# Optimization experiments

Measured on AMD Instinct MI355X. Metric: run time of the kernel, lower is better.

## Reference

```python
import jax, jax.numpy as jnp
import numpy as np

C = 256          # channels
K = 7            # kernel_size
GC = 16          # group_channels (hardcoded in module)
G = C // GC      # groups = 16
RED = 4          # reduction_ratio
PAD = (K - 1) // 2
EPS = 1e-5


def _bn(x, gamma, beta, mean, var):
    # inference-mode BatchNorm2d over channel dim (axis=1)
    inv = gamma / jnp.sqrt(var + EPS)
    return x * inv[None, :, None, None] + (beta - mean * inv)[None, :, None, None]


def setup_inputs() -> dict:
    key = jax.random.key(0)
    ks = jax.random.split(key, 8)
    cm = C // RED  # 64
    x = jax.random.normal(ks[0], (4, C, 64, 64), dtype=jnp.float32)
    w1 = jax.random.normal(ks[1], (cm, C), dtype=jnp.float32) * (1.0 / np.sqrt(C))
    bn1_gamma = jnp.abs(jax.random.normal(ks[2], (cm,), dtype=jnp.float32)) + 0.5
    bn1_beta = jax.random.normal(ks[3], (cm,), dtype=jnp.float32) * 0.1
    bn1_mean = jnp.zeros((cm,), jnp.float32)
    bn1_var = jnp.ones((cm,), jnp.float32)
    w2 = jax.random.normal(ks[4], (K * K * G, cm), dtype=jnp.float32) * (1.0 / np.sqrt(cm))
    b2 = jax.random.normal(ks[5], (K * K * G,), dtype=jnp.float32) * 0.1
    bn2_gamma = jnp.abs(jax.random.normal(ks[6], (C,), dtype=jnp.float32)) + 0.5
    bn2_beta = jax.random.normal(ks[7], (C,), dtype=jnp.float32) * 0.1
    bn2_mean = jnp.zeros((C,), jnp.float32)
    bn2_var = jnp.ones((C,), jnp.float32)
    return {"x": x, "w1": w1, "bn1_gamma": bn1_gamma, "bn1_beta": bn1_beta,
            "bn1_mean": bn1_mean, "bn1_var": bn1_var, "w2": w2, "b2": b2,
            "bn2_gamma": bn2_gamma, "bn2_beta": bn2_beta,
            "bn2_mean": bn2_mean, "bn2_var": bn2_var}


def reference(x, w1, bn1_gamma, bn1_beta, bn1_mean, bn1_var,
              w2, b2, bn2_gamma, bn2_beta, bn2_mean, bn2_var):
    b, c, h, w = x.shape
    # weight branch: 1x1 conv (no bias) -> BN -> ReLU -> 1x1 conv (bias)
    t = jnp.einsum('oc,bchw->bohw', w1, x)
    t = jax.nn.relu(_bn(t, bn1_gamma, bn1_beta, bn1_mean, bn1_var))
    wgt = jnp.einsum('oc,bchw->bohw', w2, t) + b2[None, :, None, None]
    wgt = wgt.reshape(b, G, K * K, h, w)  # per-pixel kernel per group
    # unfold x: extract KxK patches (stride 1, pad PAD), torch ordering:
    # channel slowest, kernel row, kernel col fastest
    x_pad = jnp.pad(x, ((0, 0), (0, 0), (PAD, PAD), (PAD, PAD)))
    patches = jnp.stack([x_pad[:, :, i:i + h, j:j + w]
                         for i in range(K) for j in range(K)], axis=2)  # (b,c,K2,h,w)
    patches = patches.reshape(b, G, GC, K * K, h, w)
    out = jnp.einsum('bgckhw,bgkhw->bgchw', patches, wgt).reshape(b, c, h, w)
    return jax.nn.relu(_bn(out, bn2_gamma, bn2_beta, bn2_mean, bn2_var))
```

## Files before the change

### kernel.cpp

```cpp
#include <hip/hip_runtime.h>

#define BN 4
#define C 256
#define H 64
#define W 64
#define CM 64
#define G 16
#define GC 16
#define KS 7
#define K2 49
#define PADD 3
#define EPSV 1e-5f

#define TS 16
#define HSLOT_U 388

#define W1T_OFF 0
#define B2P_OFF (W1T_OFF + C*CM)
#define S1_OFF  (B2P_OFF + G*64)
#define B1_OFF  (S1_OFF + CM)
#define S2_OFF  (B1_OFF + CM)
#define B2C_OFF (S2_OFF + C)
#define ZERO_OFF (B2C_OFF + C)
#define ABF_OFF (ZERO_OFF + 16)
#define TBF_OFF (ABF_OFF + 32768)
#define XBF_OFF (TBF_OFF + 524288)

typedef __attribute__((ext_vector_type(8))) short bf16x8;
typedef __attribute__((ext_vector_type(4))) float f32x4;

__device__ __forceinline__ uint f2bf_rne(float f) {
  uint u = __float_as_uint(f);
  return (u + 0x7fffu + ((u >> 16) & 1u)) >> 16;
}

__device__ __forceinline__ void gload_lds4(const void* g, void* l) {
  __builtin_amdgcn_global_load_lds(
      (const __attribute__((address_space(1))) void*)g,
      (__attribute__((address_space(3))) void*)l, 4, 0, 0);
}

__global__ __launch_bounds__(256) void prep_kernel(
    const float* __restrict__ w1, const float* __restrict__ w2,
    const float* __restrict__ b2,
    const float* __restrict__ g1, const float* __restrict__ be1,
    const float* __restrict__ m1, const float* __restrict__ v1,
    const float* __restrict__ g2, const float* __restrict__ be2,
    const float* __restrict__ m2, const float* __restrict__ v2,
    float* __restrict__ ws) {
  int tid = blockIdx.x * 256 + threadIdx.x;
  int nthr = gridDim.x * 256;
  for (int i = tid; i < CM * C; i += nthr) {
    int o = i / C, c = i - o * C;
    ws[W1T_OFF + c * CM + o] = w1[i];
  }
  {
    ushort* abf = (ushort*)(ws + ABF_OFF);
    for (int i = tid; i < G * 4 * 2 * 64 * 8; i += nthr) {
      int j = i & 7, lane = (i >> 3) & 63, ks = (i >> 9) & 1;
      int mt = (i >> 10) & 3, g = (i >> 12) & 15;
      int m = mt * 16 + (lane & 15);
      int o = ks * 32 + ((lane >> 4) << 3) + j;
      float v = (m < K2) ? w2[(g * K2 + m) * CM + o] : 0.f;
      abf[i] = (ushort)f2bf_rne(v);
    }
  }
  for (int i = tid; i < G * 64; i += nthr) {
    int g = i >> 6, k = i & 63;
    ws[B2P_OFF + i] = (k < K2) ? b2[g * K2 + k] : 0.f;
  }
  if (tid < CM) {
    float inv = g1[tid] * rsqrtf(v1[tid] + EPSV);
    ws[S1_OFF + tid] = inv;
    ws[B1_OFF + tid] = be1[tid] - m1[tid] * inv;
  }
  if (tid < C) {
    float inv = g2[tid] * rsqrtf(v2[tid] + EPSV);
    ws[S2_OFF + tid] = inv;
    ws[B2C_OFF + tid] = be2[tid] - m2[tid] * inv;
  }
  if (tid < 16) ws[ZERO_OFF + tid] = 0.f;
}

__global__ __launch_bounds__(256) void t_kernel(
    const float* __restrict__ x, float* __restrict__ ws) {
  __shared__ float part[4][32][64];
  int p = threadIdx.x & 63;
  int q = __builtin_amdgcn_readfirstlane(threadIdx.x >> 6);
  int y = blockIdx.x, b = blockIdx.y, oh = blockIdx.z;
  const float* __restrict__ w1T = ws + W1T_OFF + oh * 32;
  ushort* __restrict__ xbf = (ushort*)(ws + XBF_OFF);

  float acc[32];
#pragma unroll
  for (int o = 0; o < 32; ++o) acc[o] = 0.f;
  const float* __restrict__ xrow = x + (((size_t)b * C + q * 64) * H + y) * W;
#pragma unroll 2
  for (int cc = 0; cc < 64; ++cc) {
    float xv = xrow[(size_t)cc * H * W + p];
    if (oh == 0)
      xbf[(size_t)(b * C + q * 64 + cc) * (H * W) + y * W + p] = (ushort)f2bf_rne(xv);
    const float* __restrict__ wr = w1T + (q * 64 + cc) * CM;
#pragma unroll
    for (int o = 0; o < 32; ++o) acc[o] = fmaf(wr[o], xv, acc[o]);
  }
#pragma unroll
  for (int o = 0; o < 32; ++o) part[q][o][p] = acc[o];
  __syncthreads();

  int tile = (y >> 4) * 4 + (p >> 4);
  int pix = (y & 15) * 16 + (p & 15);
  const float* __restrict__ s1 = ws + S1_OFF + oh * 32;
  const float* __restrict__ b1 = ws + B1_OFF + oh * 32;
  float fv[8];
#pragma unroll
  for (int i = 0; i < 8; ++i) {
    int o = q * 8 + i;
    float s = part[0][o][p] + part[1][o][p] + part[2][o][p] + part[3][o][p];
    fv[i] = fmaxf(fmaf(s, s1[o], b1[o]), 0.f);
  }
  uint4 pk;
  pk.x = f2bf_rne(fv[0]) | (f2bf_rne(fv[1]) << 16);
  pk.y = f2bf_rne(fv[2]) | (f2bf_rne(fv[3]) << 16);
  pk.z = f2bf_rne(fv[4]) | (f2bf_rne(fv[5]) << 16);
  pk.w = f2bf_rne(fv[6]) | (f2bf_rne(fv[7]) << 16);
  ushort* tbf = (ushort*)(ws + TBF_OFF);
  size_t idx = (((size_t)(b * 16 + tile) * 256 + pix) * 64) + oh * 32 + q * 8;
  *(uint4*)(tbf + idx) = pk;
}

__global__ __launch_bounds__(256, 3) void inv_kernel(
    const float* __restrict__ ws, float* __restrict__ out) {
  __shared__ uint wgt_u[25][256];
  __shared__ uint xh[G * HSLOT_U];

  int tid = threadIdx.x;
  int lane = tid & 63;
  int wv = __builtin_amdgcn_readfirstlane(tid >> 6);
  int c16 = lane & 15, q = lane >> 4;
  int tile = blockIdx.x, g = blockIdx.y, b = blockIdx.z;
  int ty = (tile >> 2) * TS, tx = (tile & 3) * TS;
  int py = tid >> 4, pq = (tid >> 2) & 3, chq = tid & 3;

  const ushort* abf = (const ushort*)(ws + ABF_OFF);
  const ushort* tbf = (const ushort*)(ws + TBF_OFF);
  const uint* xbfu = (const uint*)(ws + XBF_OFF);

  float scv[4], bcv[4];
#pragma unroll
  for (int ci = 0; ci < 4; ++ci) {
    int ch = ci * 4 + chq;
    scv[ci] = ws[S2_OFF + g * GC + ch];
    bcv[ci] = ws[B2C_OFF + g * GC + ch];
  }

  bf16x8 afr[4][2], bfr[4][2];
  f32x4 bias[4];
#pragma unroll
  for (int mt = 0; mt < 4; ++mt) {
#pragma unroll
    for (int ks = 0; ks < 2; ++ks)
      afr[mt][ks] = *(const bf16x8*)(abf + ((g * 8 + mt * 2 + ks) * 64 + lane) * 8);
    bias[mt] = *(const f32x4*)(ws + B2P_OFF + g * 64 + mt * 16 + q * 4);
  }
#pragma unroll
  for (int nt = 0; nt < 4; ++nt) {
    int pix = wv * 64 + nt * 16 + c16;
#pragma unroll
    for (int ks = 0; ks < 2; ++ks)
      bfr[nt][ks] = *(const bf16x8*)(
          tbf + (((size_t)(b * 16 + tile) * 256 + pix) * 64 + ks * 32 + q * 8));
  }

  {
    int hofs[6];
    uint hmask = 0;
#pragma unroll
    for (int i = 0; i < 6; ++i) {
      int s = i * 64 + lane;
      int row = s >> 4, m = s & 15;
      int gy = ty - 3 + row;
      int gx0 = tx - 4 + 2 * m;
      bool v = (m < 12) && (row < 22) && ((unsigned)gy < H) && ((unsigned)gx0 < 63);
      hmask |= (uint)v << i;
      hofs[i] = gy * 32 + (gx0 >> 1);
    }
    const uint* zsrc = (const uint*)(ws + ZERO_OFF);
#pragma unroll
    for (int j = 0; j < 4; ++j) {
      int ch = wv * 4 + j;
      const uint* src_ch = xbfu + (((size_t)(b * C + g * GC + ch) * (H * W)) >> 1);
#pragma unroll
      for (int i = 0; i < 6; ++i) {
        const uint* s = ((hmask >> i) & 1u) ? (src_ch + hofs[i]) : zsrc;
        gload_lds4(s, &xh[ch * HSLOT_U + i * 64]);
      }
    }
  }

#pragma unroll
  for (int nt = 0; nt < 4; ++nt) {
    f32x4 a[4];
#pragma unroll
    for (int mt = 0; mt < 4; ++mt) a[mt] = bias[mt];
#pragma unroll
    for (int ks = 0; ks < 2; ++ks)
#pragma unroll
      for (int mt = 0; mt < 4; ++mt)
        a[mt] = __builtin_amdgcn_mfma_f32_16x16x32_bf16(afr[mt][ks], bfr[nt][ks],
                                                        a[mt], 0, 0, 0);
    int pix = wv * 64 + nt * 16 + c16;
#pragma unroll
    for (int mt = 0; mt < 4; ++mt) {
      uint lo = f2bf_rne(a[mt][0]) | (f2bf_rne(a[mt][1]) << 16);
      uint hi = f2bf_rne(a[mt][2]) | (f2bf_rne(a[mt][3]) << 16);
      int j0v = mt * 8 + q * 2;
      if (j0v < 25) wgt_u[j0v][pix] = lo;
      if (j0v + 1 < 25) wgt_u[j0v + 1][pix] = hi;
    }
  }

  asm volatile("s_waitcnt vmcnt(0) lgkmcnt(0)" ::: "memory");
  __builtin_amdgcn_s_barrier();
  __builtin_amdgcn_sched_barrier(0);

  f32x4 acc[4];
#pragma unroll
  for (int ci = 0; ci < 4; ++ci) acc[ci] = (f32x4){0.f, 0.f, 0.f, 0.f};

#pragma unroll
  for (int di = 0; di < KS; ++di) {
    const int j0 = (di * KS) >> 1;
    uint4 wq[4];
#pragma unroll
    for (int m = 0; m < 4; ++m)
      wq[m] = *(const uint4*)&wgt_u[j0 + m][py * 16 + pq * 4];
    float wf[28];
#pragma unroll
    for (int dj = 0; dj < KS; ++dj) {
      const int k = di * KS + dj;
      const int m = (k >> 1) - j0, hf = k & 1;
#pragma unroll
      for (int i = 0; i < 4; ++i) {
        uint u = (&wq[m].x)[i];
        wf[dj * 4 + i] = __uint_as_float(hf ? (u & 0xffff0000u) : (u << 16));
      }
    }
    int rowb = (py + di) * 16 + 2 * pq;
#pragma unroll
    for (int ci = 0; ci < 4; ++ci) {
      int ch = ci * 4 + chq;
      const uint* sl = &xh[ch * HSLOT_U + rowb];
      uint2 r0 = *(const uint2*)(sl);
      uint2 r1 = *(const uint2*)(sl + 2);
      uint2 r2 = *(const uint2*)(sl + 4);
      float hv[12];
      hv[1] = __uint_as_float(r0.x & 0xffff0000u);
      hv[2] = __uint_as_float(r0.y << 16);
      hv[3] = __uint_as_float(r0.y & 0xffff0000u);
      hv[4] = __uint_as_float(r1.x << 16);
      hv[5] = __uint_as_float(r1.x & 0xffff0000u);
      hv[6] = __uint_as_float(r1.y << 16);
      hv[7] = __uint_as_float(r1.y & 0xffff0000u);
      hv[8] = __uint_as_float(r2.x << 16);
      hv[9] = __uint_as_float(r2.x & 0xffff0000u);
      hv[10] = __uint_as_float(r2.y << 16);
#pragma unroll
      for (int dj = 0; dj < KS; ++dj)
#pragma unroll
        for (int i = 0; i < 4; ++i)
          acc[ci][i] = fmaf(hv[i + dj + 1], wf[dj * 4 + i], acc[ci][i]);
    }
  }

#pragma unroll
  for (int ci = 0; ci < 4; ++ci) {
    int ch = ci * 4 + chq;
    float4 o4;
    o4.x = fmaxf(fmaf(acc[ci][0], scv[ci], bcv[ci]), 0.f);
    o4.y = fmaxf(fmaf(acc[ci][1], scv[ci], bcv[ci]), 0.f);
    o4.z = fmaxf(fmaf(acc[ci][2], scv[ci], bcv[ci]), 0.f);
    o4.w = fmaxf(fmaf(acc[ci][3], scv[ci], bcv[ci]), 0.f);
    *(float4*)(out + (((size_t)b * C + g * GC + ch) * H + ty + py) * W + tx + pq * 4) = o4;
  }
}

extern "C" void kernel_launch(void* const* d_in, const int* in_sizes, int n_in,
                              void* d_out, int out_size, void* d_ws, size_t ws_size,
                              hipStream_t stream) {
  const float* x   = (const float*)d_in[0];
  const float* w1  = (const float*)d_in[1];
  const float* g1  = (const float*)d_in[2];
  const float* be1 = (const float*)d_in[3];
  const float* m1  = (const float*)d_in[4];
  const float* v1  = (const float*)d_in[5];
  const float* w2  = (const float*)d_in[6];
  const float* b2  = (const float*)d_in[7];
  const float* g2  = (const float*)d_in[8];
  const float* be2 = (const float*)d_in[9];
  const float* m2  = (const float*)d_in[10];
  const float* v2  = (const float*)d_in[11];
  float* outp = (float*)d_out;
  float* ws = (float*)d_ws;

  prep_kernel<<<dim3(64), dim3(256), 0, stream>>>(w1, w2, b2, g1, be1, m1, v1,
                                                  g2, be2, m2, v2, ws);
  t_kernel<<<dim3(H, BN, 2), dim3(256), 0, stream>>>(x, ws);
  inv_kernel<<<dim3(16, G, BN), dim3(256), 0, stream>>>(ws, outp);
}
```

Measured before the change: 51.95 us.

## Split fused involution kernel into separate bf16 cast, weight-gen, and stencil kernels

Moves the x-to-bf16 conversion out of t_kernel into a dedicated vectorized cast kernel. Splits the fused involution kernel into a weight-generation MFMA kernel that writes per-pixel kernels to global workspace, and a stencil kernel that reads them back from global instead of LDS. This frees LDS and registers in the stencil kernel for higher occupancy and removes the conditional scattered bf16 stores from t_kernel. The cost is two extra launches and a global round-trip of the generated weights of roughly 6.5 MB.

```diff
diff --git a/kernel.cpp b/kernel.cpp
--- a/kernel.cpp
+++ b/kernel.cpp
@@ -25,6 +25,7 @@
 #define ABF_OFF (ZERO_OFF + 16)
 #define TBF_OFF (ABF_OFF + 32768)
 #define XBF_OFF (TBF_OFF + 524288)
+#define WGT_OFF (XBF_OFF + 2097152)
 
 typedef __attribute__((ext_vector_type(8))) short bf16x8;
 typedef __attribute__((ext_vector_type(4))) float f32x4;
@@ -82,6 +83,19 @@
   if (tid < 16) ws[ZERO_OFF + tid] = 0.f;
 }
 
+__global__ __launch_bounds__(256) void xbf_kernel(
+    const float* __restrict__ x, float* __restrict__ ws) {
+  size_t i = ((size_t)blockIdx.x * 256 + threadIdx.x) * 8;
+  const float4* src = (const float4*)(x + i);
+  float4 a = src[0], b = src[1];
+  uint4 pk;
+  pk.x = f2bf_rne(a.x) | (f2bf_rne(a.y) << 16);
+  pk.y = f2bf_rne(a.z) | (f2bf_rne(a.w) << 16);
+  pk.z = f2bf_rne(b.x) | (f2bf_rne(b.y) << 16);
+  pk.w = f2bf_rne(b.z) | (f2bf_rne(b.w) << 16);
+  *(uint4*)((ushort*)(ws + XBF_OFF) + i) = pk;
+}
+
 __global__ __launch_bounds__(256) void t_kernel(
     const float* __restrict__ x, float* __restrict__ ws) {
   __shared__ float part[4][32][64];
@@ -89,7 +103,6 @@
   int q = __builtin_amdgcn_readfirstlane(threadIdx.x >> 6);
   int y = blockIdx.x, b = blockIdx.y, oh = blockIdx.z;
   const float* __restrict__ w1T = ws + W1T_OFF + oh * 32;
-  ushort* __restrict__ xbf = (ushort*)(ws + XBF_OFF);
 
   float acc[32];
 #pragma unroll
@@ -98,8 +111,6 @@
 #pragma unroll 2
   for (int cc = 0; cc < 64; ++cc) {
     float xv = xrow[(size_t)cc * H * W + p];
-    if (oh == 0)
-      xbf[(size_t)(b * C + q * 64 + cc) * (H * W) + y * W + p] = (ushort)f2bf_rne(xv);
     const float* __restrict__ wr = w1T + (q * 64 + cc) * CM;
 #pragma unroll
     for (int o = 0; o < 32; ++o) acc[o] = fmaf(wr[o], xv, acc[o]);
@@ -129,30 +140,16 @@
   *(uint4*)(tbf + idx) = pk;
 }
 
-__global__ __launch_bounds__(256, 3) void inv_kernel(
-    const float* __restrict__ ws, float* __restrict__ out) {
-  __shared__ uint wgt_u[25][256];
-  __shared__ uint xh[G * HSLOT_U];
-
+__global__ __launch_bounds__(256) void wgt_kernel(
+    const float* __restrict__ ws, float* __restrict__ wsw) {
   int tid = threadIdx.x;
   int lane = tid & 63;
   int wv = __builtin_amdgcn_readfirstlane(tid >> 6);
   int c16 = lane & 15, q = lane >> 4;
   int tile = blockIdx.x, g = blockIdx.y, b = blockIdx.z;
-  int ty = (tile >> 2) * TS, tx = (tile & 3) * TS;
-  int py = tid >> 4, pq = (tid >> 2) & 3, chq = tid & 3;
 
   const ushort* abf = (const ushort*)(ws + ABF_OFF);
   const ushort* tbf = (const ushort*)(ws + TBF_OFF);
-  const uint* xbfu = (const uint*)(ws + XBF_OFF);
-
-  float scv[4], bcv[4];
-#pragma unroll
-  for (int ci = 0; ci < 4; ++ci) {
-    int ch = ci * 4 + chq;
-    scv[ci] = ws[S2_OFF + g * GC + ch];
-    bcv[ci] = ws[B2C_OFF + g * GC + ch];
-  }
 
   bf16x8 afr[4][2], bfr[4][2];
   f32x4 bias[4];
@@ -171,6 +168,45 @@
       bfr[nt][ks] = *(const bf16x8*)(
           tbf + (((size_t)(b * 16 + tile) * 256 + pix) * 64 + ks * 32 + q * 8));
   }
+
+  uint* wgt_g = (uint*)(wsw + WGT_OFF) + ((size_t)((b * 16 + tile) * 16 + g) * 25) * 256;
+#pragma unroll
+  for (int nt = 0; nt < 4; ++nt) {
+    f32x4 a[4];
+#pragma unroll
+    for (int mt = 0; mt < 4; ++mt) a[mt] = bias[mt];
+#pragma unroll
+    for (int ks = 0; ks < 2; ++ks)
+#pragma unroll
+      for (int mt = 0; mt < 4; ++mt)
+        a[mt] = __builtin_amdgcn_mfma_f32_16x16x32_bf16(afr[mt][ks], bfr[nt][ks],
+                                                        a[mt], 0, 0, 0);
+    int pix = wv * 64 + nt * 16 + c16;
+#pragma unroll
+    for (int mt = 0; mt < 4; ++mt) {
+      uint lo = f2bf_rne(a[mt][0]) | (f2bf_rne(a[mt][1]) << 16);
+      uint hi = f2bf_rne(a[mt][2]) | (f2bf_rne(a[mt][3]) << 16);
+      int j0v = mt * 8 + q * 2;
+      if (j0v < 25) wgt_g[j0v * 256 + pix] = lo;
+      if (j0v + 1 < 25) wgt_g[(j0v + 1) * 256 + pix] = hi;
+    }
+  }
+}
+
+__global__ __launch_bounds__(256) void stencil_kernel(
+    const float* __restrict__ ws, float* __restrict__ out) {
+  __shared__ uint xh[G * HSLOT_U];
+
+  int tid = threadIdx.x;
+  int lane = tid & 63;
+  int wv = __builtin_amdgcn_readfirstlane(tid >> 6);
+  int tile = blockIdx.x, g = blockIdx.y, b = blockIdx.z;
+  int ty = (tile >> 2) * TS, tx = (tile & 3) * TS;
+  int py = tid >> 4, pq = (tid >> 2) & 3, chq = tid & 3;
+
+  const uint* xbfu = (const uint*)(ws + XBF_OFF);
+  const uint* wgt_g = (const uint*)(ws + WGT_OFF) +
+                      ((size_t)((b * 16 + tile) * 16 + g) * 25) * 256;
 
   {
     int hofs[6];
@@ -198,32 +234,19 @@
     }
   }
 
-#pragma unroll
-  for (int nt = 0; nt < 4; ++nt) {
-    f32x4 a[4];
-#pragma unroll
-    for (int mt = 0; mt < 4; ++mt) a[mt] = bias[mt];
-#pragma unroll
-    for (int ks = 0; ks < 2; ++ks)
-#pragma unroll
-      for (int mt = 0; mt < 4; ++mt)
-        a[mt] = __builtin_amdgcn_mfma_f32_16x16x32_bf16(afr[mt][ks], bfr[nt][ks],
-                                                        a[mt], 0, 0, 0);
-    int pix = wv * 64 + nt * 16 + c16;
-#pragma unroll
-    for (int mt = 0; mt < 4; ++mt) {
-      uint lo = f2bf_rne(a[mt][0]) | (f2bf_rne(a[mt][1]) << 16);
-      uint hi = f2bf_rne(a[mt][2]) | (f2bf_rne(a[mt][3]) << 16);
-      int j0v = mt * 8 + q * 2;
-      if (j0v < 25) wgt_u[j0v][pix] = lo;
-      if (j0v + 1 < 25) wgt_u[j0v + 1][pix] = hi;
-    }
-  }
-
-  asm volatile("s_waitcnt vmcnt(0) lgkmcnt(0)" ::: "memory");
+  float scv[4], bcv[4];
+#pragma unroll
+  for (int ci = 0; ci < 4; ++ci) {
+    int ch = ci * 4 + chq;
+    scv[ci] = ws[S2_OFF + g * GC + ch];
+    bcv[ci] = ws[B2C_OFF + g * GC + ch];
+  }
+
+  asm volatile("s_waitcnt vmcnt(0)" ::: "memory");
   __builtin_amdgcn_s_barrier();
   __builtin_amdgcn_sched_barrier(0);
 
+  int pix0 = py * 16 + pq * 4;
   f32x4 acc[4];
 #pragma unroll
   for (int ci = 0; ci < 4; ++ci) acc[ci] = (f32x4){0.f, 0.f, 0.f, 0.f};
@@ -234,7 +257,7 @@
     uint4 wq[4];
 #pragma unroll
     for (int m = 0; m < 4; ++m)
-      wq[m] = *(const uint4*)&wgt_u[j0 + m][py * 16 + pq * 4];
+      wq[m] = *(const uint4*)(wgt_g + (j0 + m) * 256 + pix0);
     float wf[28];
 #pragma unroll
     for (int dj = 0; dj < KS; ++dj) {
@@ -305,6 +328,8 @@
 
   prep_kernel<<<dim3(64), dim3(256), 0, stream>>>(w1, w2, b2, g1, be1, m1, v1,
                                                   g2, be2, m2, v2, ws);
+  xbf_kernel<<<dim3(BN * C * H * W / 2048), dim3(256), 0, stream>>>(x, ws);
   t_kernel<<<dim3(H, BN, 2), dim3(256), 0, stream>>>(x, ws);
-  inv_kernel<<<dim3(16, G, BN), dim3(256), 0, stream>>>(ws, outp);
-}
+  wgt_kernel<<<dim3(16, G, BN), dim3(256), 0, stream>>>(ws, ws);
+  stencil_kernel<<<dim3(16, G, BN), dim3(256), 0, stream>>>(ws, outp);
+}
```

Measured after the change: 57.35 us. 10.4% more time.

## Double-buffer channel halo staging in inv_kernel and move x bf16 conversion to prep

Applied to the files above, without the earlier changes.

The inv_kernel now stages its x halo four channels at a time into two LDS buffers and overlaps the next stage's global-to-LDS loads with compute on the current one. This cuts LDS use so occupancy can rise to four blocks per CU, and pads the strides to reduce bank conflicts. The bf16 conversion of x moves out of t_kernel into a widened 2048-block prep_kernel that does vectorized loads. The cost is extra barriers and waitcnt phases in inv_kernel, plus a larger prep launch that reads x one more time.

```diff
diff --git a/kernel.cpp b/kernel.cpp
--- a/kernel.cpp
+++ b/kernel.cpp
@@ -13,7 +13,8 @@
 #define EPSV 1e-5f
 
 #define TS 16
-#define HSLOT_U 388
+#define HSTRIDE_U 389
+#define WSTRIDE 260
 
 #define W1T_OFF 0
 #define B2P_OFF (W1T_OFF + C*CM)
@@ -41,6 +42,7 @@
 }
 
 __global__ __launch_bounds__(256) void prep_kernel(
+    const float* __restrict__ x,
     const float* __restrict__ w1, const float* __restrict__ w2,
     const float* __restrict__ b2,
     const float* __restrict__ g1, const float* __restrict__ be1,
@@ -50,6 +52,19 @@
     float* __restrict__ ws) {
   int tid = blockIdx.x * 256 + threadIdx.x;
   int nthr = gridDim.x * 256;
+
+  {
+    size_t i = (size_t)tid * 8;
+    const float4* src = (const float4*)(x + i);
+    float4 a = src[0], b = src[1];
+    uint4 pk;
+    pk.x = f2bf_rne(a.x) | (f2bf_rne(a.y) << 16);
+    pk.y = f2bf_rne(a.z) | (f2bf_rne(a.w) << 16);
+    pk.z = f2bf_rne(b.x) | (f2bf_rne(b.y) << 16);
+    pk.w = f2bf_rne(b.z) | (f2bf_rne(b.w) << 16);
+    *(uint4*)((ushort*)(ws + XBF_OFF) + i) = pk;
+  }
+
   for (int i = tid; i < CM * C; i += nthr) {
     int o = i / C, c = i - o * C;
     ws[W1T_OFF + c * CM + o] = w1[i];
@@ -89,7 +104,6 @@
   int q = __builtin_amdgcn_readfirstlane(threadIdx.x >> 6);
   int y = blockIdx.x, b = blockIdx.y, oh = blockIdx.z;
   const float* __restrict__ w1T = ws + W1T_OFF + oh * 32;
-  ushort* __restrict__ xbf = (ushort*)(ws + XBF_OFF);
 
   float acc[32];
 #pragma unroll
@@ -98,8 +112,6 @@
 #pragma unroll 2
   for (int cc = 0; cc < 64; ++cc) {
     float xv = xrow[(size_t)cc * H * W + p];
-    if (oh == 0)
-      xbf[(size_t)(b * C + q * 64 + cc) * (H * W) + y * W + p] = (ushort)f2bf_rne(xv);
     const float* __restrict__ wr = w1T + (q * 64 + cc) * CM;
 #pragma unroll
     for (int o = 0; o < 32; ++o) acc[o] = fmaf(wr[o], xv, acc[o]);
@@ -129,10 +141,10 @@
   *(uint4*)(tbf + idx) = pk;
 }
 
-__global__ __launch_bounds__(256, 3) void inv_kernel(
+__global__ __launch_bounds__(256, 4) void inv_kernel(
     const float* __restrict__ ws, float* __restrict__ out) {
-  __shared__ uint wgt_u[25][256];
-  __shared__ uint xh[G * HSLOT_U];
+  __shared__ uint wgt_u[25][WSTRIDE];
+  __shared__ uint xh[2 * 4 * HSTRIDE_U];
 
   int tid = threadIdx.x;
   int lane = tid & 63;
@@ -148,10 +160,9 @@
 
   float scv[4], bcv[4];
 #pragma unroll
-  for (int ci = 0; ci < 4; ++ci) {
-    int ch = ci * 4 + chq;
-    scv[ci] = ws[S2_OFF + g * GC + ch];
-    bcv[ci] = ws[B2C_OFF + g * GC + ch];
+  for (int p = 0; p < 4; ++p) {
+    scv[p] = ws[S2_OFF + g * GC + p * 4 + chq];
+    bcv[p] = ws[B2C_OFF + g * GC + p * 4 + chq];
   }
 
   bf16x8 afr[4][2], bfr[4][2];
@@ -172,31 +183,33 @@
           tbf + (((size_t)(b * 16 + tile) * 256 + pix) * 64 + ks * 32 + q * 8));
   }
 
-  {
-    int hofs[6];
-    uint hmask = 0;
-#pragma unroll
-    for (int i = 0; i < 6; ++i) {
-      int s = i * 64 + lane;
-      int row = s >> 4, m = s & 15;
-      int gy = ty - 3 + row;
-      int gx0 = tx - 4 + 2 * m;
-      bool v = (m < 12) && (row < 22) && ((unsigned)gy < H) && ((unsigned)gx0 < 63);
-      hmask |= (uint)v << i;
-      hofs[i] = gy * 32 + (gx0 >> 1);
-    }
-    const uint* zsrc = (const uint*)(ws + ZERO_OFF);
-#pragma unroll
-    for (int j = 0; j < 4; ++j) {
-      int ch = wv * 4 + j;
-      const uint* src_ch = xbfu + (((size_t)(b * C + g * GC + ch) * (H * W)) >> 1);
-#pragma unroll
-      for (int i = 0; i < 6; ++i) {
-        const uint* s = ((hmask >> i) & 1u) ? (src_ch + hofs[i]) : zsrc;
-        gload_lds4(s, &xh[ch * HSLOT_U + i * 64]);
-      }
-    }
-  }
+  int hofs[6];
+  uint hmask = 0;
+#pragma unroll
+  for (int i = 0; i < 6; ++i) {
+    int s = i * 64 + lane;
+    int row = s >> 4, m = s & 15;
+    int gy = ty - 3 + row;
+    int gx0 = tx - 4 + 2 * m;
+    bool v = (m < 12) && (row < 22) && ((unsigned)gy < H) && ((unsigned)gx0 < 63);
+    hmask |= (uint)v << i;
+    hofs[i] = gy * 32 + (gx0 >> 1);
+  }
+  const uint* zsrc = (const uint*)(ws + ZERO_OFF);
+  const uint* xgb = xbfu + (((size_t)(b * C + g * GC) * (H * W)) >> 1);
+
+#define STAGE(CH, BUF) do {                                                \
+    const uint* src_ = xgb + ((size_t)(CH) * (H * W) >> 1);                \
+    uint* dst_ = &xh[((BUF) * 4 + ((CH) & 3)) * HSTRIDE_U];                \
+    _Pragma("unroll")                                                      \
+    for (int i_ = 0; i_ < 6; ++i_) {                                       \
+      const uint* s_ = ((hmask >> i_) & 1u) ? (src_ + hofs[i_]) : zsrc;    \
+      gload_lds4(s_, dst_ + i_ * 64);                                      \
+    }                                                                      \
+  } while (0)
+
+  STAGE(wv, 0);
+  STAGE(4 + wv, 1);
 
 #pragma unroll
   for (int nt = 0; nt < 4; ++nt) {
@@ -220,37 +233,28 @@
     }
   }
 
-  asm volatile("s_waitcnt vmcnt(0) lgkmcnt(0)" ::: "memory");
-  __builtin_amdgcn_s_barrier();
-  __builtin_amdgcn_sched_barrier(0);
-
-  f32x4 acc[4];
-#pragma unroll
-  for (int ci = 0; ci < 4; ++ci) acc[ci] = (f32x4){0.f, 0.f, 0.f, 0.f};
-
-#pragma unroll
-  for (int di = 0; di < KS; ++di) {
-    const int j0 = (di * KS) >> 1;
-    uint4 wq[4];
-#pragma unroll
-    for (int m = 0; m < 4; ++m)
-      wq[m] = *(const uint4*)&wgt_u[j0 + m][py * 16 + pq * 4];
-    float wf[28];
-#pragma unroll
-    for (int dj = 0; dj < KS; ++dj) {
-      const int k = di * KS + dj;
-      const int m = (k >> 1) - j0, hf = k & 1;
-#pragma unroll
-      for (int i = 0; i < 4; ++i) {
-        uint u = (&wq[m].x)[i];
-        wf[dj * 4 + i] = __uint_as_float(hf ? (u & 0xffff0000u) : (u << 16));
+  auto phase = [&](int bufI, int p) {
+    f32x4 acc = {0.f, 0.f, 0.f, 0.f};
+#pragma unroll
+    for (int di = 0; di < KS; ++di) {
+      const int j0 = (di * KS) >> 1;
+      uint4 wq[4];
+#pragma unroll
+      for (int m = 0; m < 4; ++m)
+        wq[m] = *(const uint4*)&wgt_u[j0 + m][py * 16 + pq * 4];
+      float wf[28];
+#pragma unroll
+      for (int dj = 0; dj < KS; ++dj) {
+        const int k = di * KS + dj;
+        const int m = (k >> 1) - j0, hf = k & 1;
+#pragma unroll
+        for (int i = 0; i < 4; ++i) {
+          uint u = (&wq[m].x)[i];
+          wf[dj * 4 + i] = __uint_as_float(hf ? (u & 0xffff0000u) : (u << 16));
+        }
       }
-    }
-    int rowb = (py + di) * 16 + 2 * pq;
-#pragma unroll
-    for (int ci = 0; ci < 4; ++ci) {
-      int ch = ci * 4 + chq;
-      const uint* sl = &xh[ch * HSLOT_U + rowb];
+      int rowb = (py + di) * 16 + 2 * pq;
+      const uint* sl = &xh[(bufI * 4 + chq) * HSTRIDE_U + rowb];
       uint2 r0 = *(const uint2*)(sl);
       uint2 r1 = *(const uint2*)(sl + 2);
       uint2 r2 = *(const uint2*)(sl + 4);
@@ -269,20 +273,45 @@
       for (int dj = 0; dj < KS; ++dj)
 #pragma unroll
         for (int i = 0; i < 4; ++i)
-          acc[ci][i] = fmaf(hv[i + dj + 1], wf[dj * 4 + i], acc[ci][i]);
+          acc[i] = fmaf(hv[i + dj + 1], wf[dj * 4 + i], acc[i]);
     }
-  }
-
-#pragma unroll
-  for (int ci = 0; ci < 4; ++ci) {
-    int ch = ci * 4 + chq;
+    int ch = p * 4 + chq;
     float4 o4;
-    o4.x = fmaxf(fmaf(acc[ci][0], scv[ci], bcv[ci]), 0.f);
-    o4.y = fmaxf(fmaf(acc[ci][1], scv[ci], bcv[ci]), 0.f);
-    o4.z = fmaxf(fmaf(acc[ci][2], scv[ci], bcv[ci]), 0.f);
-    o4.w = fmaxf(fmaf(acc[ci][3], scv[ci], bcv[ci]), 0.f);
+    o4.x = fmaxf(fmaf(acc[0], scv[p], bcv[p]), 0.f);
+    o4.y = fmaxf(fmaf(acc[1], scv[p], bcv[p]), 0.f);
+    o4.z = fmaxf(fmaf(acc[2], scv[p], bcv[p]), 0.f);
+    o4.w = fmaxf(fmaf(acc[3], scv[p], bcv[p]), 0.f);
     *(float4*)(out + (((size_t)b * C + g * GC + ch) * H + ty + py) * W + tx + pq * 4) = o4;
-  }
+  };
+
+  asm volatile("s_waitcnt vmcnt(6) lgkmcnt(0)" ::: "memory");
+  __builtin_amdgcn_s_barrier();
+  __builtin_amdgcn_sched_barrier(0);
+  phase(0, 0);
+
+  asm volatile("s_waitcnt lgkmcnt(0)" ::: "memory");
+  __builtin_amdgcn_s_barrier();
+  __builtin_amdgcn_sched_barrier(0);
+  STAGE(8 + wv, 0);
+  asm volatile("s_waitcnt vmcnt(6) lgkmcnt(0)" ::: "memory");
+  __builtin_amdgcn_s_barrier();
+  __builtin_amdgcn_sched_barrier(0);
+  phase(1, 1);
+
+  asm volatile("s_waitcnt lgkmcnt(0)" ::: "memory");
+  __builtin_amdgcn_s_barrier();
+  __builtin_amdgcn_sched_barrier(0);
+  STAGE(12 + wv, 1);
+  asm volatile("s_waitcnt vmcnt(6) lgkmcnt(0)" ::: "memory");
+  __builtin_amdgcn_s_barrier();
+  __builtin_amdgcn_sched_barrier(0);
+  phase(0, 2);
+
+  asm volatile("s_waitcnt vmcnt(0) lgkmcnt(0)" ::: "memory");
+  __builtin_amdgcn_s_barrier();
+  __builtin_amdgcn_sched_barrier(0);
+  phase(1, 3);
+#undef STAGE
 }
 
 extern "C" void kernel_launch(void* const* d_in, const int* in_sizes, int n_in,
@@ -303,8 +332,8 @@
   float* outp = (float*)d_out;
   float* ws = (float*)d_ws;
 
-  prep_kernel<<<dim3(64), dim3(256), 0, stream>>>(w1, w2, b2, g1, be1, m1, v1,
-                                                  g2, be2, m2, v2, ws);
+  prep_kernel<<<dim3(2048), dim3(256), 0, stream>>>(x, w1, w2, b2, g1, be1, m1, v1,
+                                                    g2, be2, m2, v2, ws);
   t_kernel<<<dim3(H, BN, 2), dim3(256), 0, stream>>>(x, ws);
   inv_kernel<<<dim3(16, G, BN), dim3(256), 0, stream>>>(ws, outp);
 }
```

Result: slower. 73.72 us (+41.9%).

## Move x bf16 conversion into prep kernel and compact padded LDS halo layout

Applied to the files above, without the earlier changes.

The x-to-bf16 conversion leaves t_kernel, where it ran as a scalar store per element in the oh==0 blocks. It now runs in the widened prep_kernel (2048 blocks), which converts 8 floats per thread with vector loads and stores. The inv_kernel halo tile is packed at 12 words per row instead of 16, so it needs 5 global-to-LDS loads per channel instead of 6. The LDS strides for the weights and halo are padded (260, 321) to reduce bank conflicts. The MFMA operand loads are reordered and the manual waitcnt/barrier becomes __syncthreads. In exchange, prep_kernel becomes a heavier serial step, and the odd halo stride may leave the 8-byte LDS reads misaligned.

```diff
diff --git a/kernel.cpp b/kernel.cpp
--- a/kernel.cpp
+++ b/kernel.cpp
@@ -13,7 +13,8 @@
 #define EPSV 1e-5f
 
 #define TS 16
-#define HSLOT_U 388
+#define HSTRIDE_U 321
+#define WSTRIDE 260
 
 #define W1T_OFF 0
 #define B2P_OFF (W1T_OFF + C*CM)
@@ -41,6 +42,7 @@
 }
 
 __global__ __launch_bounds__(256) void prep_kernel(
+    const float* __restrict__ x,
     const float* __restrict__ w1, const float* __restrict__ w2,
     const float* __restrict__ b2,
     const float* __restrict__ g1, const float* __restrict__ be1,
@@ -50,6 +52,19 @@
     float* __restrict__ ws) {
   int tid = blockIdx.x * 256 + threadIdx.x;
   int nthr = gridDim.x * 256;
+
+  {
+    size_t i = (size_t)tid * 8;
+    const float4* src = (const float4*)(x + i);
+    float4 a = src[0], b = src[1];
+    uint4 pk;
+    pk.x = f2bf_rne(a.x) | (f2bf_rne(a.y) << 16);
+    pk.y = f2bf_rne(a.z) | (f2bf_rne(a.w) << 16);
+    pk.z = f2bf_rne(b.x) | (f2bf_rne(b.y) << 16);
+    pk.w = f2bf_rne(b.z) | (f2bf_rne(b.w) << 16);
+    *(uint4*)((ushort*)(ws + XBF_OFF) + i) = pk;
+  }
+
   for (int i = tid; i < CM * C; i += nthr) {
     int o = i / C, c = i - o * C;
     ws[W1T_OFF + c * CM + o] = w1[i];
@@ -89,7 +104,6 @@
   int q = __builtin_amdgcn_readfirstlane(threadIdx.x >> 6);
   int y = blockIdx.x, b = blockIdx.y, oh = blockIdx.z;
   const float* __restrict__ w1T = ws + W1T_OFF + oh * 32;
-  ushort* __restrict__ xbf = (ushort*)(ws + XBF_OFF);
 
   float acc[32];
 #pragma unroll
@@ -98,8 +112,6 @@
 #pragma unroll 2
   for (int cc = 0; cc < 64; ++cc) {
     float xv = xrow[(size_t)cc * H * W + p];
-    if (oh == 0)
-      xbf[(size_t)(b * C + q * 64 + cc) * (H * W) + y * W + p] = (ushort)f2bf_rne(xv);
     const float* __restrict__ wr = w1T + (q * 64 + cc) * CM;
 #pragma unroll
     for (int o = 0; o < 32; ++o) acc[o] = fmaf(wr[o], xv, acc[o]);
@@ -131,8 +143,8 @@
 
 __global__ __launch_bounds__(256, 3) void inv_kernel(
     const float* __restrict__ ws, float* __restrict__ out) {
-  __shared__ uint wgt_u[25][256];
-  __shared__ uint xh[G * HSLOT_U];
+  __shared__ uint wgt_u[25][WSTRIDE];
+  __shared__ uint xh[G * HSTRIDE_U];
 
   int tid = threadIdx.x;
   int lane = tid & 63;
@@ -146,6 +158,23 @@
   const ushort* tbf = (const ushort*)(ws + TBF_OFF);
   const uint* xbfu = (const uint*)(ws + XBF_OFF);
 
+  bf16x8 afr[4][2], bfr[4][2];
+  f32x4 bias[4];
+#pragma unroll
+  for (int nt = 0; nt < 4; ++nt) {
+    int pix = wv * 64 + nt * 16 + c16;
+#pragma unroll
+    for (int ks = 0; ks < 2; ++ks)
+      bfr[nt][ks] = *(const bf16x8*)(
+          tbf + (((size_t)(b * 16 + tile) * 256 + pix) * 64 + ks * 32 + q * 8));
+  }
+#pragma unroll
+  for (int mt = 0; mt < 4; ++mt) {
+#pragma unroll
+    for (int ks = 0; ks < 2; ++ks)
+      afr[mt][ks] = *(const bf16x8*)(abf + ((g * 8 + mt * 2 + ks) * 64 + lane) * 8);
+    bias[mt] = *(const f32x4*)(ws + B2P_OFF + g * 64 + mt * 16 + q * 4);
+  }
   float scv[4], bcv[4];
 #pragma unroll
   for (int ci = 0; ci < 4; ++ci) {
@@ -154,46 +183,30 @@
     bcv[ci] = ws[B2C_OFF + g * GC + ch];
   }
 
-  bf16x8 afr[4][2], bfr[4][2];
-  f32x4 bias[4];
-#pragma unroll
-  for (int mt = 0; mt < 4; ++mt) {
-#pragma unroll
-    for (int ks = 0; ks < 2; ++ks)
-      afr[mt][ks] = *(const bf16x8*)(abf + ((g * 8 + mt * 2 + ks) * 64 + lane) * 8);
-    bias[mt] = *(const f32x4*)(ws + B2P_OFF + g * 64 + mt * 16 + q * 4);
-  }
-#pragma unroll
-  for (int nt = 0; nt < 4; ++nt) {
-    int pix = wv * 64 + nt * 16 + c16;
-#pragma unroll
-    for (int ks = 0; ks < 2; ++ks)
-      bfr[nt][ks] = *(const bf16x8*)(
-          tbf + (((size_t)(b * 16 + tile) * 256 + pix) * 64 + ks * 32 + q * 8));
-  }
-
   {
-    int hofs[6];
+    int hofs[5];
     uint hmask = 0;
 #pragma unroll
-    for (int i = 0; i < 6; ++i) {
-      int s = i * 64 + lane;
-      int row = s >> 4, m = s & 15;
+    for (int i = 0; i < 5; ++i) {
+      int idx = i * 64 + lane;
+      int row = idx / 12, m = idx - row * 12;
       int gy = ty - 3 + row;
       int gx0 = tx - 4 + 2 * m;
-      bool v = (m < 12) && (row < 22) && ((unsigned)gy < H) && ((unsigned)gx0 < 63);
+      bool v = (idx < 264) && ((unsigned)gy < H) && ((unsigned)gx0 < 64);
       hmask |= (uint)v << i;
       hofs[i] = gy * 32 + (gx0 >> 1);
     }
     const uint* zsrc = (const uint*)(ws + ZERO_OFF);
+    const uint* xgb = xbfu + (((size_t)(b * C + g * GC) * (H * W)) >> 1);
 #pragma unroll
     for (int j = 0; j < 4; ++j) {
       int ch = wv * 4 + j;
-      const uint* src_ch = xbfu + (((size_t)(b * C + g * GC + ch) * (H * W)) >> 1);
-#pragma unroll
-      for (int i = 0; i < 6; ++i) {
+      const uint* src_ch = xgb + ((size_t)ch * (H * W) >> 1);
+      uint* dst = &xh[ch * HSTRIDE_U];
+#pragma unroll
+      for (int i = 0; i < 5; ++i) {
         const uint* s = ((hmask >> i) & 1u) ? (src_ch + hofs[i]) : zsrc;
-        gload_lds4(s, &xh[ch * HSLOT_U + i * 64]);
+        gload_lds4(s, dst + i * 64);
       }
     }
   }
@@ -220,9 +233,7 @@
     }
   }
 
-  asm volatile("s_waitcnt vmcnt(0) lgkmcnt(0)" ::: "memory");
-  __builtin_amdgcn_s_barrier();
-  __builtin_amdgcn_sched_barrier(0);
+  __syncthreads();
 
   f32x4 acc[4];
 #pragma unroll
@@ -246,11 +257,11 @@
         wf[dj * 4 + i] = __uint_as_float(hf ? (u & 0xffff0000u) : (u << 16));
       }
     }
-    int rowb = (py + di) * 16 + 2 * pq;
+    int rowb = (py + di) * 12 + 2 * pq;
 #pragma unroll
     for (int ci = 0; ci < 4; ++ci) {
       int ch = ci * 4 + chq;
-      const uint* sl = &xh[ch * HSLOT_U + rowb];
+      const uint* sl = &xh[ch * HSTRIDE_U + rowb];
       uint2 r0 = *(const uint2*)(sl);
       uint2 r1 = *(const uint2*)(sl + 2);
       uint2 r2 = *(const uint2*)(sl + 4);
@@ -303,8 +314,8 @@
   float* outp = (float*)d_out;
   float* ws = (float*)d_ws;
 
-  prep_kernel<<<dim3(64), dim3(256), 0, stream>>>(w1, w2, b2, g1, be1, m1, v1,
-                                                  g2, be2, m2, v2, ws);
+  prep_kernel<<<dim3(2048), dim3(256), 0, stream>>>(x, w1, w2, b2, g1, be1, m1, v1,
+                                                    g2, be2, m2, v2, ws);
   t_kernel<<<dim3(H, BN, 2), dim3(256), 0, stream>>>(x, ws);
   inv_kernel<<<dim3(16, G, BN), dim3(256), 0, stream>>>(ws, outp);
 }
```

After: 72.51 us. 39.6% more time.
